# Kernel optimization log

Hardware: AMD Instinct MI355X
Metric: run time of the kernel (lower is better)

## Reference

```python
import jax, jax.numpy as jnp
import numpy as np

B, T, E = 2, 2048, 2048
H, NOPE, ROPE, VD, KVR, DR = 16, 64, 32, 64, 256, 2
QKD = NOPE + ROPE  # 96
LOWR = KVR // 4    # hypernet low_rank=4 -> 64


def _rope_angles(position, dim):
    # freqs_cis angles: pos * 10000^(-2i/dim), matching torch rotary with theta=10000
    inv = jnp.exp(jnp.arange(0, dim, 2, dtype=jnp.float32) * (-jnp.log(jnp.float32(10000.0)) / dim))
    return position.astype(jnp.float32)[..., None] * inv  # (1, T, dim//2)


def _apply_rotary(x, ang):
    # x: (B,T,H,D); pairs are consecutive elements (view_as_complex semantics)
    x2 = x.reshape(x.shape[:-1] + (-1, 2))
    c = jnp.cos(ang)[:, :, None, :]
    s = jnp.sin(ang)[:, :, None, :]
    xr, xi = x2[..., 0], x2[..., 1]
    return jnp.stack([xr * c - xi * s, xr * s + xi * c], axis=-1).reshape(x.shape)


def _layernorm(x, g, b, eps=1e-5):
    m = jnp.mean(x, axis=-1, keepdims=True)
    v = jnp.var(x, axis=-1, keepdims=True)
    return (x - m) * jax.lax.rsqrt(v + eps) * g + b


def _sinusoid_pe(t, d):
    pos = jnp.arange(t, dtype=jnp.float32)[:, None]
    div = jnp.exp(jnp.arange(0, d, 2, dtype=jnp.float32) * (-jnp.log(jnp.float32(10000.0)) / d))
    pe = jnp.zeros((t, d), dtype=jnp.float32)
    pe = pe.at[:, 0::2].set(jnp.sin(pos * div)).at[:, 1::2].set(jnp.cos(pos * div))
    return pe


def setup_inputs() -> dict:
    key = jax.random.key(0)
    ks = jax.random.split(key, 16)
    sd = 0.02
    return {
        "query": jax.random.normal(ks[0], (B, T, E), jnp.float32),
        "key": jax.random.normal(ks[1], (B, T, E), jnp.float32),
        "value": jax.random.normal(ks[2], (B, T, E), jnp.float32),
        "position": jnp.arange(T, dtype=jnp.int32)[None, :],
        # weights stored transposed for right-multiply (x @ W)
        "wq": jax.random.normal(ks[3], (E, H * QKD), jnp.float32) * sd,
        "wkv_a": jax.random.normal(ks[4], (E, KVR + ROPE), jnp.float32) * sd,
        "kv_gamma": jnp.ones((KVR,), jnp.float32),
        "kv_beta": jnp.zeros((KVR,), jnp.float32),
        # torch layout (H*(NOPE+VD), KVR) kept for faithful view(H,-1,KVR) absorb
        "wkv_b": jax.random.normal(ks[5], (H * (NOPE + VD), KVR), jnp.float32) * sd,
        "wo": jax.random.normal(ks[6], (H * VD, E), jnp.float32) * sd,
        "fc_c_w": jax.random.normal(ks[7], (KVR, LOWR), jnp.float32) * sd,
        "fc_c_b": jnp.zeros((LOWR,), jnp.float32),
        "fc_p_w": jax.random.normal(ks[8], (KVR, LOWR), jnp.float32) * sd,
        "fc_p_b": jnp.zeros((LOWR,), jnp.float32),
    }


def reference(query, key, value, position, wq, wkv_a, kv_gamma, kv_beta, wkv_b, wo,
              fc_c_w, fc_c_b, fc_p_w, fc_p_b):
    bsz, seqlen, _ = query.shape
    # queries: low-rank-free path (q_lora_rank=0)
    q = (query @ wq).reshape(bsz, seqlen, H, QKD)
    q_nope, q_pe = q[..., :NOPE], q[..., NOPE:]
    ang = _rope_angles(position, ROPE)  # (1, T, ROPE//2)
    q_pe = _apply_rotary(q_pe, ang[:, -seqlen:])
    # key/value latent projection
    kv_all = key @ wkv_a  # (B, T, KVR+ROPE)
    kv, k_pe = kv_all[..., :KVR], kv_all[..., KVR:]
    k_pe = _apply_rotary(k_pe[:, :, None, :], ang)[:, :, 0, :]  # (B, T, ROPE)
    kv_norm = _layernorm(kv, kv_gamma, kv_beta)  # (B, T, KVR)
    # hypernetwork temporal downsampling weights (train path, T_input=kv_norm)
    t = -(-seqlen // DR)
    C = jnp.repeat(_sinusoid_pe(t, KVR), DR, axis=0)[:seqlen]  # (T, KVR)
    C2 = C @ fc_c_w + fc_c_b           # (T, LOWR)
    P2 = kv_norm @ fc_p_w + fc_p_b     # (B, T, LOWR)
    W = jax.nn.sigmoid(jnp.einsum('tc,bsc->bts', C2, P2))  # (B, T, T)
    idx = jnp.arange(seqlen)
    chunk = idx // DR
    # chunk mask: cumulative within-chunk causal accumulation
    zero_mask = ((chunk[:, None] == chunk[None, :]) & (idx[None, :] <= idx[:, None])).astype(query.dtype)
    kv_t = jnp.einsum('bts,bsc->btc', W * zero_mask, kv_norm)  # (B, T, KVR)
    # stride-aware causal mask: attend completed chunk-end slots + own in-progress slot
    allowed = (idx[None, :] == idx[:, None]) | ((idx[None, :] < idx[:, None]) & (((idx[None, :] + 1) % DR) == 0))
    attn_mask = jnp.where(allowed, jnp.float32(0.0), jnp.float32(-1e30))
    # absorbed MLA attention
    wb = wkv_b.reshape(H, NOPE + VD, KVR)
    q_abs = jnp.einsum('bshd,hdc->bshc', q_nope, wb[:, :NOPE])  # (B, S, H, KVR)
    scores = (jnp.einsum('bshc,btc->bsht', q_abs, kv_t)
              + jnp.einsum('bshr,btr->bsht', q_pe, k_pe)) * (QKD ** -0.5)
    scores = scores + attn_mask[None, :, None, :]
    attn = jax.nn.softmax(scores, axis=-1)
    x = jnp.einsum('bsht,btc->bshc', attn, kv_t)
    x = jnp.einsum('bshc,hdc->bshd', x, wb[:, NOPE:])  # (B, S, H, VD)
    return x.reshape(bsz, seqlen, H * VD) @ wo
```

## Files before the change

kernel.cpp:

```cpp
#include <hip/hip_runtime.h>
#include <stddef.h>

typedef unsigned short u16;
typedef unsigned short u16x8 __attribute__((ext_vector_type(8)));
typedef short s16x8 __attribute__((ext_vector_type(8)));
typedef float f32x4 __attribute__((ext_vector_type(4)));

#define B_ 2
#define T_ 2048
#define E_ 2048
#define H_ 16

__device__ inline float us2f(u16 u){
  unsigned int i = ((unsigned int)u) << 16;
  return __builtin_bit_cast(float, i);
}
__device__ inline u16 f2us(float f){
  unsigned int x = __builtin_bit_cast(unsigned int, f);
  unsigned int r = (x + 0x7fffu + ((x >> 16) & 1u)) >> 16;
  return (u16)r;
}
__device__ inline f32x4 mfma32(s16x8 a, s16x8 b, f32x4 c){
  return __builtin_amdgcn_mfma_f32_16x16x32_bf16(a, b, c, 0, 0, 0);
}
__device__ inline s16x8 ld8(const u16* p){
  return __builtin_bit_cast(s16x8, *(const u16x8*)p);
}
__device__ inline void gload_lds16(const u16* g, u16* l){
  __builtin_amdgcn_global_load_lds(
      (const __attribute__((address_space(1))) unsigned int*)(g),
      (__attribute__((address_space(3))) unsigned int*)(l), 16, 0, 0);
}

__global__ __launch_bounds__(256) void prep_weights(
    const float* __restrict__ wq, const float* __restrict__ wkva,
    const float* __restrict__ wo, const float* __restrict__ wkvb,
    u16* __restrict__ wqT, u16* __restrict__ wkvaT, u16* __restrict__ woT,
    u16* __restrict__ wkvbB)
{
  __shared__ float tile[32][33];
  const int bid = blockIdx.x;
  const int tid = threadIdx.x;
  if (bid < 5696) {
    const float* in; u16* out; int R, C, bx, by;
    if (bid < 3072)      { in = wq;   out = wqT;   R = 2048; C = 1536; bx = bid % 48;          by = bid / 48; }
    else if (bid < 3648) { in = wkva; out = wkvaT; R = 2048; C = 288;  bx = (bid-3072) % 9;    by = (bid-3072) / 9; }
    else                 { in = wo;   out = woT;   R = 1024; C = 2048; bx = (bid-3648) % 64;   by = (bid-3648) / 64; }
    int tx = tid & 31, ty = tid >> 5;
    int c0 = bx * 32, r0 = by * 32;
    for (int i = ty; i < 32; i += 8){
      int r = r0 + i, c = c0 + tx;
      tile[i][tx] = (r < R && c < C) ? in[(size_t)r * C + c] : 0.f;
    }
    __syncthreads();
    for (int i = ty; i < 32; i += 8){
      int c = c0 + i, r = r0 + tx;
      if (c < C && r < R) out[(size_t)c * R + r] = f2us(tile[tx][i]);
    }
  } else {
    int i = (bid - 5696) * 1024 + tid * 4;
    f32x4 v = *(const f32x4*)(wkvb + i);
    wkvbB[i]   = f2us(v[0]); wkvbB[i+1] = f2us(v[1]);
    wkvbB[i+2] = f2us(v[2]); wkvbB[i+3] = f2us(v[3]);
  }
}

__global__ __launch_bounds__(256) void cvt2_f32_bf16(const float* __restrict__ a,
    const float* __restrict__ b, u16* __restrict__ oa, u16* __restrict__ ob, int n_each)
{
  int idx = (blockIdx.x * 256 + threadIdx.x) * 4;
  const float* in; u16* out; int i;
  if (idx < n_each){ in = a; out = oa; i = idx; }
  else             { in = b; out = ob; i = idx - n_each; }
  if (i + 3 < n_each){
    f32x4 v = *(const f32x4*)(in + i);
    out[i]   = f2us(v[0]); out[i+1] = f2us(v[1]);
    out[i+2] = f2us(v[2]); out[i+3] = f2us(v[3]);
  }
}

template<int A_F32, int OUT_F32>
__global__ __launch_bounds__(256) void gemm_bt(const void* __restrict__ Ap,
    const u16* __restrict__ Bt, void* __restrict__ Cp, int M, int N, int K)
{
  __shared__ __align__(16) u16 As[64][40];
  __shared__ __align__(16) u16 Bs[64][40];
  const int tid  = threadIdx.x;
  const int lane = tid & 63;
  const int wid  = tid >> 6;
  const int quad = lane >> 4;
  const int col  = lane & 15;
  const int bm = blockIdx.y * 64;
  const int bn = blockIdx.x * 64;
  const int lr = tid >> 2;
  const int lc = (tid & 3) * 8;
  const int waveM = wid >> 1, waveN = wid & 1;

  f32x4 acc[2][2];
  for (int i = 0; i < 2; ++i)
    for (int j = 0; j < 2; ++j)
      acc[i][j] = (f32x4){0.f, 0.f, 0.f, 0.f};

  const u16x8 zero8 = {0,0,0,0,0,0,0,0};
  const bool bok = (bn + lr) < N;
  const u16*   arow16 = (const u16*)Ap   + (size_t)(bm + lr) * K + lc;
  const float* arow32 = (const float*)Ap + (size_t)(bm + lr) * K + lc;
  const u16* brow = Bt + (size_t)(bn + lr) * K + lc;

  for (int kk = 0; kk < K; kk += 32) {
    u16x8 av;
    if (A_F32) {
      f32x4 a0 = *(const f32x4*)(arow32 + kk);
      f32x4 a1 = *(const f32x4*)(arow32 + kk + 4);
      av[0]=f2us(a0[0]); av[1]=f2us(a0[1]); av[2]=f2us(a0[2]); av[3]=f2us(a0[3]);
      av[4]=f2us(a1[0]); av[5]=f2us(a1[1]); av[6]=f2us(a1[2]); av[7]=f2us(a1[3]);
    } else {
      av = *(const u16x8*)(arow16 + kk);
    }
    u16x8 bv = bok ? *(const u16x8*)(brow + kk) : zero8;
    __syncthreads();
    *(u16x8*)&As[lr][lc] = av;
    *(u16x8*)&Bs[lr][lc] = bv;
    __syncthreads();
    s16x8 af0 = ld8(&As[waveM*32 + col][quad*8]);
    s16x8 af1 = ld8(&As[waveM*32 + 16 + col][quad*8]);
    s16x8 bf0 = ld8(&Bs[waveN*32 + col][quad*8]);
    s16x8 bf1 = ld8(&Bs[waveN*32 + 16 + col][quad*8]);
    acc[0][0] = mfma32(af0, bf0, acc[0][0]);
    acc[0][1] = mfma32(af0, bf1, acc[0][1]);
    acc[1][0] = mfma32(af1, bf0, acc[1][0]);
    acc[1][1] = mfma32(af1, bf1, acc[1][1]);
  }
  for (int am = 0; am < 2; ++am)
    for (int bnn = 0; bnn < 2; ++bnn)
      for (int i = 0; i < 4; ++i) {
        int r = bm + waveM*32 + am*16 + quad*4 + i;
        int c = bn + waveN*32 + bnn*16 + col;
        if (c < N){
          if (OUT_F32) ((float*)Cp)[(size_t)r * N + c] = acc[am][bnn][i];
          else         ((u16*)Cp)[(size_t)r * N + c]   = f2us(acc[am][bnn][i]);
        }
      }
}

template<int OUT_F32>
__global__ __launch_bounds__(256) void gemm128(const u16* __restrict__ A,
    const u16* __restrict__ Bt, void* __restrict__ Cp, int M, int N, int K, int gx)
{
  __shared__ __align__(16) u16 As[2 * 128 * 32];
  __shared__ __align__(16) u16 Bs[2 * 128 * 32];
  const int lin = blockIdx.x;
  const int cpx = gridDim.x >> 3;
  const int swz = (lin & 7) * cpx + (lin >> 3);
  const int bxi = swz % gx;
  const int byi = swz / gx;
  const int tid  = threadIdx.x;
  const int lane = tid & 63;
  const int wid  = tid >> 6;
  const int quad = lane >> 4;
  const int col  = lane & 15;
  const int bm = byi * 128;
  const int bn = bxi * 128;
  const int waveM = wid >> 1, waveN = wid & 1;

  const int srow = wid * 16 + (lane >> 2);
  const int scol = (lane & 3) * 8;
  const u16* ga = A  + (size_t)(bm + srow) * K + scol;
  const u16* gb = Bt + (size_t)(bn + srow) * K + scol;
  const size_t rowskip = (size_t)64 * K;

  f32x4 acc[4][4] = {};
  const int nt = K >> 5;

  auto STAGE = [&](int buf, int kk){
    u16* la = &As[buf * 4096 + wid * 512];
    u16* lb = &Bs[buf * 4096 + wid * 512];
    gload_lds16(ga + kk,           la);
    gload_lds16(ga + rowskip + kk, la + 2048);
    gload_lds16(gb + kk,           lb);
    gload_lds16(gb + rowskip + kk, lb + 2048);
  };

  STAGE(0, 0);
  asm volatile("s_waitcnt vmcnt(0)" ::: "memory");
  __builtin_amdgcn_s_barrier();
  __builtin_amdgcn_sched_barrier(0);

  int cur = 0;
  for (int it = 0; it < nt; ++it){
    if (it + 1 < nt) STAGE(cur ^ 1, (it + 1) * 32);
    const u16* as = &As[cur * 4096];
    const u16* bs = &Bs[cur * 4096];
    s16x8 af[4], bf[4];
#pragma unroll
    for (int i = 0; i < 4; ++i) af[i] = ld8(&as[(waveM*64 + i*16 + col) * 32 + quad*8]);
#pragma unroll
    for (int i = 0; i < 4; ++i) bf[i] = ld8(&bs[(waveN*64 + i*16 + col) * 32 + quad*8]);
#pragma unroll
    for (int i = 0; i < 4; ++i)
#pragma unroll
      for (int j = 0; j < 4; ++j)
        acc[i][j] = mfma32(af[i], bf[j], acc[i][j]);
    asm volatile("s_waitcnt lgkmcnt(0)" ::: "memory");
    if (it + 1 < nt)
      asm volatile("s_waitcnt vmcnt(0)" ::: "memory");
    __builtin_amdgcn_s_barrier();
    __builtin_amdgcn_sched_barrier(0);
    cur ^= 1;
  }
#pragma unroll
  for (int i = 0; i < 4; ++i)
#pragma unroll
    for (int j = 0; j < 4; ++j)
#pragma unroll
      for (int r = 0; r < 4; ++r) {
        int row = bm + waveM*64 + i*16 + quad*4 + r;
        int c   = bn + waveN*64 + j*16 + col;
        if (OUT_F32) ((float*)Cp)[(size_t)row * N + c] = acc[i][j][r];
        else         ((u16*)Cp)[(size_t)row * N + c]   = f2us(acc[i][j][r]);
      }
}

__global__ __launch_bounds__(256) void gemm128_sk(const u16* __restrict__ A,
    const u16* __restrict__ Bt, u16* __restrict__ qp,
    int M, int N, int K, int Klen)
{
  __shared__ __align__(16) u16 As[2 * 128 * 32];
  __shared__ __align__(16) u16 Bs[2 * 128 * 32];
  const int lin = blockIdx.x;
  const int swz = (lin & 7) * 96 + (lin >> 3);
  const int kh  = swz / 384;
  const int rem = swz % 384;
  const int byi = rem / 12;
  const int bxi = rem % 12;
  const int tid  = threadIdx.x;
  const int lane = tid & 63;
  const int wid  = tid >> 6;
  const int quad = lane >> 4;
  const int col  = lane & 15;
  const int bm = byi * 128;
  const int bn = bxi * 128;
  const int waveM = wid >> 1, waveN = wid & 1;

  const int srow = wid * 16 + (lane >> 2);
  const int scol = (lane & 3) * 8;
  const u16* ga = A  + (size_t)(bm + srow) * K + kh * Klen + scol;
  const u16* gb = Bt + (size_t)(bn + srow) * K + kh * Klen + scol;
  const size_t rowskip = (size_t)64 * K;
  u16* Cp = qp + (size_t)kh * M * N;

  f32x4 acc[4][4] = {};
  const int nt = Klen >> 5;

  auto STAGE = [&](int buf, int kk){
    u16* la = &As[buf * 4096 + wid * 512];
    u16* lb = &Bs[buf * 4096 + wid * 512];
    gload_lds16(ga + kk,           la);
    gload_lds16(ga + rowskip + kk, la + 2048);
    gload_lds16(gb + kk,           lb);
    gload_lds16(gb + rowskip + kk, lb + 2048);
  };

  STAGE(0, 0);
  asm volatile("s_waitcnt vmcnt(0)" ::: "memory");
  __builtin_amdgcn_s_barrier();
  __builtin_amdgcn_sched_barrier(0);

  int cur = 0;
  for (int it = 0; it < nt; ++it){
    if (it + 1 < nt) STAGE(cur ^ 1, (it + 1) * 32);
    const u16* as = &As[cur * 4096];
    const u16* bs = &Bs[cur * 4096];
    s16x8 af[4], bf[4];
#pragma unroll
    for (int i = 0; i < 4; ++i) af[i] = ld8(&as[(waveM*64 + i*16 + col) * 32 + quad*8]);
#pragma unroll
    for (int i = 0; i < 4; ++i) bf[i] = ld8(&bs[(waveN*64 + i*16 + col) * 32 + quad*8]);
#pragma unroll
    for (int i = 0; i < 4; ++i)
#pragma unroll
      for (int j = 0; j < 4; ++j)
        acc[i][j] = mfma32(af[i], bf[j], acc[i][j]);
    asm volatile("s_waitcnt lgkmcnt(0)" ::: "memory");
    if (it + 1 < nt)
      asm volatile("s_waitcnt vmcnt(0)" ::: "memory");
    __builtin_amdgcn_s_barrier();
    __builtin_amdgcn_sched_barrier(0);
    cur ^= 1;
  }
#pragma unroll
  for (int i = 0; i < 4; ++i)
#pragma unroll
    for (int j = 0; j < 4; ++j)
#pragma unroll
      for (int r = 0; r < 4; ++r) {
        int row = bm + waveM*64 + i*16 + quad*4 + r;
        int c   = bn + waveN*64 + j*16 + col;
        Cp[(size_t)row * N + c] = f2us(acc[i][j][r]);
      }
}

__global__ __launch_bounds__(256) void qsplit(const u16* __restrict__ qp,
    const int* __restrict__ pos, u16* __restrict__ qh)
{
  const size_t PS = 4096ull * 1536;
  int idx = blockIdx.x * 256 + threadIdx.x;
  if (idx >= B_*T_*H_*12) return;
  int c    = idx % 12;
  int rest = idx / 12;
  int h    = rest & 15;
  int row  = rest >> 4;
  int t    = row & (T_ - 1);
  int b    = row >> 11;
  size_t off = (size_t)row * 1536 + h * 96 + c * 8;
  u16x8 v0 = *(const u16x8*)(qp + off);
  u16x8 v1 = *(const u16x8*)(qp + PS + off);
  u16x8 v;
  if (c < 8) {
#pragma unroll
    for (int k = 0; k < 8; ++k) v[k] = f2us(us2f(v0[k]) + us2f(v1[k]));
  } else {
    int i0 = (c - 8) * 4;
    float pp = (float)pos[t];
#pragma unroll
    for (int k = 0; k < 4; ++k){
      int i = i0 + k;
      float ang = pp * __expf((float)(2*i) * -0.28782313657f);
      float cs = __cosf(ang), sn = __sinf(ang);
      float xr = us2f(v0[2*k])   + us2f(v1[2*k]);
      float xi = us2f(v0[2*k+1]) + us2f(v1[2*k+1]);
      v[2*k]   = f2us(xr * cs - xi * sn);
      v[2*k+1] = f2us(xr * sn + xi * cs);
    }
  }
  u16* dst = qh + ((size_t)(b * 16 + h) * T_ + t) * 96;
  *(u16x8*)(dst + c * 8) = v;
}

__global__ __launch_bounds__(256) void ln_p2_rope(
    const u16* __restrict__ kvall, const float* __restrict__ gamma,
    const float* __restrict__ beta, const float* __restrict__ fcpw,
    const float* __restrict__ fcpb, const int* __restrict__ pos,
    u16* __restrict__ kvn, float* __restrict__ P2, u16* __restrict__ kpe)
{
  const int row = blockIdx.x;
  if (row >= B_ * T_) return;
  const int tid = threadIdx.x;
  const int lane = tid & 63, wid = tid >> 6;
  __shared__ float kvs[256];
  __shared__ float part[256];
  __shared__ float redS[4], redS2[4];
  const u16* src = kvall + (size_t)row * 288;
  float v = us2f(src[tid]);
  float s1 = v, s2 = v * v;
  for (int off = 1; off < 64; off <<= 1){
    s1 += __shfl_xor(s1, off);
    s2 += __shfl_xor(s2, off);
  }
  if (lane == 0){ redS[wid] = s1; redS2[wid] = s2; }
  __syncthreads();
  float S  = redS[0] + redS[1] + redS[2] + redS[3];
  float Q  = redS2[0] + redS2[1] + redS2[2] + redS2[3];
  float mean = S * (1.f / 256.f);
  float var  = Q * (1.f / 256.f) - mean * mean;
  float rstd = rsqrtf(var + 1e-5f);
  float xn = (v - mean) * rstd * gamma[tid] + beta[tid];
  kvs[tid] = xn;
  kvn[(size_t)row * 256 + tid] = f2us(xn);
  __syncthreads();
  {
    int oc = tid & 63, pp = tid >> 6;
    float acc = 0.f;
#pragma unroll 8
    for (int c = pp * 64; c < pp * 64 + 64; ++c)
      acc += kvs[c] * fcpw[c * 64 + oc];
    part[tid] = acc;
  }
  __syncthreads();
  if (tid < 64) {
    P2[(size_t)row * 64 + tid] = fcpb[tid] + part[tid] + part[64 + tid]
                               + part[128 + tid] + part[192 + tid];
  } else if (tid < 80) {
    int i = tid - 64;
    int t = row & (T_ - 1);
    float ang = (float)pos[t] * __expf((float)(2*i) * -0.28782313657f);
    float c = __cosf(ang), s = __sinf(ang);
    float xr = us2f(src[256 + 2*i]);
    float xi = us2f(src[257 + 2*i]);
    kpe[(size_t)row * 32 + 2*i]     = f2us(xr * c - xi * s);
    kpe[(size_t)row * 32 + 2*i + 1] = f2us(xr * s + xi * c);
  }
}

__global__ __launch_bounds__(256) void c2_kernel(const float* __restrict__ fccw,
    const float* __restrict__ fccb, float* __restrict__ C2)
{
  const int t = blockIdx.x, tid = threadIdx.x;
  __shared__ float pe[256];
  __shared__ float part[256];
  float p = (float)(t >> 1);
  if (tid < 128){
    float div = __expf((float)(2*tid) * -0.03597789207f);
    float a = p * div;
    pe[2*tid]   = __sinf(a);
    pe[2*tid+1] = __cosf(a);
  }
  __syncthreads();
  {
    int oc = tid & 63, pp = tid >> 6;
    float acc = 0.f;
#pragma unroll 8
    for (int c = pp * 64; c < pp * 64 + 64; ++c)
      acc += pe[c] * fccw[c * 64 + oc];
    part[tid] = acc;
  }
  __syncthreads();
  if (tid < 64)
    C2[t * 64 + tid] = fccb[tid] + part[tid] + part[64 + tid]
                     + part[128 + tid] + part[192 + tid];
}

__global__ __launch_bounds__(64) void kvt_kernel(const float* __restrict__ C2,
    const float* __restrict__ P2, const u16* __restrict__ kvn, u16* __restrict__ kvt)
{
  const int row = blockIdx.x;
  if (row >= B_ * T_) return;
  const int lane = threadIdx.x;
  const int t = row & (T_ - 1);
  float c2v = C2[t * 64 + lane];
  float da = c2v * P2[(size_t)row * 64 + lane];
  for (int off = 1; off < 64; off <<= 1) da += __shfl_xor(da, off);
  float wtt = 1.f / (1.f + __expf(-da));
  const bool odd = (t & 1);
  float wts = 0.f;
  if (odd){
    float db = c2v * P2[(size_t)(row - 1) * 64 + lane];
    for (int off = 1; off < 64; off <<= 1) db += __shfl_xor(db, off);
    wts = 1.f / (1.f + __expf(-db));
  }
  for (int c = lane; c < 256; c += 64){
    float val = wtt * us2f(kvn[(size_t)row * 256 + c]);
    if (odd) val += wts * us2f(kvn[(size_t)(row - 1) * 256 + c]);
    kvt[(size_t)row * 256 + c] = f2us(val);
  }
}

__global__ __launch_bounds__(256) void vtkc_kernel(const u16* __restrict__ kvb,
    const u16* __restrict__ kpe, u16* __restrict__ Vt, u16* __restrict__ Kc)
{
  __shared__ __align__(16) u16 tile[64][72];
  const int tid = threadIdx.x;
  if (blockIdx.x < 512) {
    const int bid = blockIdx.x;
    const int jt = bid & 15;
    const int h  = (bid >> 4) & 15;
    const int b  = bid >> 8;
    const int jl = tid >> 2;
    const int dseg = (tid & 3) * 16;
    const int j0 = jt * 64;
    {
      int s_ = 2 * (j0 + jl) + 1;
      const u16* src = kvb + ((size_t)(b * T_ + s_)) * 2048 + h * 128 + 64 + dseg;
      *(u16x8*)&tile[jl][dseg]     = *(const u16x8*)(src);
      *(u16x8*)&tile[jl][dseg + 8] = *(const u16x8*)(src + 8);
    }
    __syncthreads();
    const int dl = tid >> 2;
    const int jseg = (tid & 3) * 16;
    u16* dst = Vt + ((size_t)(b * 16 + h) * 64 + dl) * 1024 + j0 + jseg;
    u16x8 o;
    for (int r = 0; r < 8; ++r) o[r] = tile[jseg + r][dl];
    *(u16x8*)dst = o;
    for (int r = 0; r < 8; ++r) o[r] = tile[jseg + 8 + r][dl];
    *(u16x8*)(dst + 8) = o;
  } else {
    int idx = (blockIdx.x - 512) * 256 + tid;
    int c  = idx % 12;
    int j  = (idx / 12) & 1023;
    int bh = idx / (12 * 1024);
    if (bh >= B_ * H_) return;
    int b = bh >> 4, h = bh & 15;
    int t = 2 * j + 1;
    u16x8 v;
    if (c < 8) v = *(const u16x8*)(kvb + ((size_t)(b * T_ + t)) * 2048 + h * 128 + c * 8);
    else       v = *(const u16x8*)(kpe + ((size_t)(b * T_ + t)) * 32 + (c - 8) * 8);
    int kl = j & 63;
    int cs = (c & 12) | ((c & 3) ^ ((kl >> 1) & 3));
    *(u16x8*)(Kc + ((size_t)bh * 1024 + j) * 96 + cs * 8) = v;
  }
}

__global__ __launch_bounds__(256) void attn_kernel(
    const u16* __restrict__ qh, const u16* __restrict__ kvb,
    const u16* __restrict__ kpe, const u16* __restrict__ Kc,
    const u16* __restrict__ Vt, u16* __restrict__ xout)
{
  __shared__ __align__(16) u16 Ks[64 * 96];
  __shared__ __align__(16) u16 Vs[64][72];
  __shared__ __align__(16) u16 pbufA[4][16 * 72];
  const int tid  = threadIdx.x;
  const int wid  = tid >> 6;
  const int lane = tid & 63;
  const int quad = lane >> 4;
  const int col  = lane & 15;
  const int qt   = 31 - (blockIdx.x >> 5);
  const int bh   = blockIdx.x & 31;
  const int b    = bh >> 4;
  const int h    = bh & 15;
  u16* pbuf = pbufA[wid];
  const float scale = 0.10206207262f;
  const u16* KcH = Kc + (size_t)bh * 1024 * 96;
  const u16* VtH = Vt + (size_t)bh * 64 * 1024;
  const int t0 = qt * 64 + wid * 16;
  const int qo = (quad * 8) ^ (((col >> 1) & 3) << 3);

  s16x8 aq0, aq1, aq2;
  {
    const u16* qrow = qh + ((size_t)bh * T_ + t0 + col) * 96;
    aq0 = ld8(qrow + quad * 8);
    aq1 = ld8(qrow + 32 + quad * 8);
    aq2 = ld8(qrow + 64 + quad * 8);
  }
  float sself;
  {
    const int t = t0 + col;
    const u16* qrow = qh + ((size_t)bh * T_ + t) * 96;
    const u16* ka = kvb + ((size_t)(b * T_ + t)) * 2048 + h * 128;
    const u16* kp = kpe + ((size_t)(b * T_ + t)) * 32;
    float a = 0.f;
#pragma unroll
    for (int c = 0; c < 8; ++c){
      u16x8 qv = *(const u16x8*)(qrow + c * 8);
      u16x8 kv = *(const u16x8*)(ka + c * 8);
#pragma unroll
      for (int jj = 0; jj < 8; ++jj) a += us2f(qv[jj]) * us2f(kv[jj]);
    }
#pragma unroll
    for (int c = 0; c < 4; ++c){
      u16x8 qv = *(const u16x8*)(qrow + 64 + c * 8);
      u16x8 kv = *(const u16x8*)(kp + c * 8);
#pragma unroll
      for (int jj = 0; jj < 8; ++jj) a += us2f(qv[jj]) * us2f(kv[jj]);
    }
    sself = a * scale;
  }
  float es[4], lacc[4];
  f32x4 O[4];
#pragma unroll
  for (int i = 0; i < 4; ++i){
    es[i] = __expf(__shfl(sself, quad * 4 + i));
    lacc[i] = 0.f;
  }
#pragma unroll
  for (int nt = 0; nt < 4; ++nt)
#pragma unroll
    for (int i = 0; i < 4; ++i){
      int t = t0 + quad * 4 + i;
      O[nt][i] = es[i] * us2f(kvb[((size_t)(b * T_ + t)) * 2048 + h * 128 + 64 + nt * 16 + col]);
    }

  const int nb = (qt * 32 + 94) >> 6;
  for (int blk = 0; blk < nb; ++blk) {
    const int jb = blk * 64;
    __syncthreads();
    {
      const u16* gk = KcH + (size_t)jb * 96 + (wid * 3) * 512 + lane * 8;
      u16* lk = &Ks[(wid * 3) * 512];
#pragma unroll
      for (int k = 0; k < 3; ++k)
        gload_lds16(gk + k * 512, lk + k * 512);
      int d = tid >> 2, c4 = tid & 3;
      const u16* gv = VtH + (size_t)d * 1024 + jb + c4 * 16;
      u16* lv = &Vs[d][c4 * 16];
      *(u16x8*)(lv)     = *(const u16x8*)(gv);
      *(u16x8*)(lv + 8) = *(const u16x8*)(gv + 8);
    }
    __syncthreads();
#pragma unroll
    for (int cc = 0; cc < 2; ++cc){
      const u16* k0 = &Ks[(cc * 32 + col) * 96];
      const u16* k1 = k0 + 16 * 96;
      f32x4 s0 = {0,0,0,0}, s1 = {0,0,0,0};
      s0 = mfma32(aq0, ld8(k0 + qo), s0);
      s0 = mfma32(aq1, ld8(k0 + 32 + qo), s0);
      s0 = mfma32(aq2, ld8(k0 + 64 + qo), s0);
      s1 = mfma32(aq0, ld8(k1 + qo), s1);
      s1 = mfma32(aq1, ld8(k1 + 32 + qo), s1);
      s1 = mfma32(aq2, ld8(k1 + 64 + qo), s1);
      int key0 = jb + cc * 32 + col;
#pragma unroll
      for (int i = 0; i < 4; ++i){
        int lim = (t0 + quad * 4 + i) >> 1;
        float p0 = (key0 < lim)      ? __expf(s0[i] * scale) : 0.f;
        float p1 = (key0 + 16 < lim) ? __expf(s1[i] * scale) : 0.f;
        lacc[i] += p0 + p1;
        pbuf[(quad * 4 + i) * 72 + cc * 32 + col]      = f2us(p0);
        pbuf[(quad * 4 + i) * 72 + cc * 32 + 16 + col] = f2us(p1);
      }
    }
    asm volatile("s_waitcnt lgkmcnt(0)" ::: "memory");
    __builtin_amdgcn_sched_barrier(0);
#pragma unroll
    for (int cc = 0; cc < 2; ++cc){
      s16x8 pf = ld8(&pbuf[col * 72 + cc * 32 + quad * 8]);
#pragma unroll
      for (int nt = 0; nt < 4; ++nt)
        O[nt] = mfma32(pf, ld8(&Vs[nt * 16 + col][cc * 32 + quad * 8]), O[nt]);
    }
  }
#pragma unroll
  for (int i = 0; i < 4; ++i){
    float l = lacc[i];
    l += __shfl_xor(l, 1);
    l += __shfl_xor(l, 2);
    l += __shfl_xor(l, 4);
    l += __shfl_xor(l, 8);
    lacc[i] = es[i] + l;
  }
#pragma unroll
  for (int nt = 0; nt < 4; ++nt)
#pragma unroll
    for (int i = 0; i < 4; ++i){
      int t = t0 + quad * 4 + i;
      xout[((size_t)(b * T_ + t)) * 1024 + h * 64 + nt * 16 + col] = f2us(O[nt][i] / lacc[i]);
    }
}

extern "C" void kernel_launch(void* const* d_in, const int* in_sizes, int n_in,
                              void* d_out, int out_size, void* d_ws, size_t ws_size,
                              hipStream_t stream)
{
  (void)in_sizes; (void)n_in; (void)out_size; (void)ws_size;
  const float* query = (const float*)d_in[0];
  const float* key_  = (const float*)d_in[1];
  const int*   pos   = (const int*)d_in[3];
  const float* wq    = (const float*)d_in[4];
  const float* wkva  = (const float*)d_in[5];
  const float* gamma = (const float*)d_in[6];
  const float* beta  = (const float*)d_in[7];
  const float* wkvb  = (const float*)d_in[8];
  const float* wo    = (const float*)d_in[9];
  const float* fccw  = (const float*)d_in[10];
  const float* fccb  = (const float*)d_in[11];
  const float* fcpw  = (const float*)d_in[12];
  const float* fcpb  = (const float*)d_in[13];

  char* p = (char*)d_ws;
  auto alloc = [&](size_t bytes) -> void* {
    void* r = (void*)p;
    p += (bytes + 255) & ~(size_t)255;
    return r;
  };
  u16* wqT    = (u16*)alloc(1536ull * 2048 * 2);
  u16* wkvaT  = (u16*)alloc(288ull  * 2048 * 2);
  u16* woT    = (u16*)alloc(2048ull * 1024 * 2);
  u16* wkvbB  = (u16*)alloc(2048ull * 256 * 2);
  u16* queryB = (u16*)alloc(4096ull * 2048 * 2);
  u16* keyB   = (u16*)alloc(4096ull * 2048 * 2);
  u16* qp     = (u16*)alloc(2ull * 4096 * 1536 * 2);
  u16* qh     = (u16*)alloc(65536ull * 96 * 2);
  u16* kvall  = (u16*)alloc(4096ull * 288 * 2);
  u16* kvn    = (u16*)alloc(4096ull * 256 * 2);
  u16* kpe    = (u16*)alloc(4096ull * 32 * 2);
  float* P2   = (float*)alloc(4096ull * 64 * 4);
  float* C2   = (float*)alloc(2048ull * 64 * 4);
  u16* kvt    = (u16*)alloc(4096ull * 256 * 2);
  u16* kvb    = (u16*)alloc(4096ull * 2048 * 2);
  char* q8 = (char*)qp;
  u16* Kc = (u16*)q8;
  u16* Vt = (u16*)(q8 + ((32ull*1024*96*2 + 255) & ~255ull));
  u16* x  = (u16*)(q8 + ((32ull*1024*96*2 + 255) & ~255ull)
                      + ((2048ull*1024*2   + 255) & ~255ull));

  prep_weights<<<6208, 256, 0, stream>>>(wq, wkva, wo, wkvb, wqT, wkvaT, woT, wkvbB);
  cvt2_f32_bf16<<<16384, 256, 0, stream>>>(query, key_, queryB, keyB, 4096 * 2048);

  gemm128_sk<<<768, 256, 0, stream>>>(queryB, wqT, qp, 4096, 1536, 2048, 1024);
  gemm_bt<0,0><<<dim3(5, 64), 256, 0, stream>>>(keyB, wkvaT, kvall, 4096, 288, 2048);

  qsplit<<<3072, 256, 0, stream>>>(qp, pos, qh);
  ln_p2_rope<<<4096, 256, 0, stream>>>(kvall, gamma, beta, fcpw, fcpb, pos, kvn, P2, kpe);
  c2_kernel<<<2048, 256, 0, stream>>>(fccw, fccb, C2);
  kvt_kernel<<<4096, 64, 0, stream>>>(C2, P2, kvn, kvt);

  gemm128<0><<<512, 256, 0, stream>>>(kvt, wkvbB, kvb, 4096, 2048, 256, 16);
  vtkc_kernel<<<2048, 256, 0, stream>>>(kvb, kpe, Vt, Kc);
  attn_kernel<<<1024, 256, 0, stream>>>(qh, kvb, kpe, Kc, Vt, x);

  gemm128<1><<<512, 256, 0, stream>>>(x, woT, d_out, 4096, 2048, 1024, 16);
}
```

Before: 347.2 us.

## Merge independent prep, projection and mid-stage kernels into combined launches

Independent kernels are merged into fewer launches by dispatching on block index. Weight prep joins the query/key conversion, the Q split-K GEMM joins the small kv_a GEMM, and qsplit, LayerNorm/P2/RoPE and C2 share one kernel. kvt_kernel now packs four rows per 256-thread block. This cuts launch overhead and lets small, under-filled kernels overlap on the GPU, at the cost of heterogeneous blocks sharing resource limits such as LDS sized for the largest branch.

```diff
diff --git a/kernel.cpp b/kernel.cpp
--- a/kernel.cpp
+++ b/kernel.cpp
@@ -32,11 +32,12 @@
       (__attribute__((address_space(3))) unsigned int*)(l), 16, 0, 0);
 }
 
-__global__ __launch_bounds__(256) void prep_weights(
+__global__ __launch_bounds__(256) void prep_cvt(
     const float* __restrict__ wq, const float* __restrict__ wkva,
     const float* __restrict__ wo, const float* __restrict__ wkvb,
+    const float* __restrict__ query, const float* __restrict__ key_,
     u16* __restrict__ wqT, u16* __restrict__ wkvaT, u16* __restrict__ woT,
-    u16* __restrict__ wkvbB)
+    u16* __restrict__ wkvbB, u16* __restrict__ queryB, u16* __restrict__ keyB)
 {
   __shared__ float tile[32][33];
   const int bid = blockIdx.x;
@@ -57,90 +58,149 @@
       int c = c0 + i, r = r0 + tx;
       if (c < C && r < R) out[(size_t)c * R + r] = f2us(tile[tx][i]);
     }
-  } else {
+  } else if (bid < 6208) {
     int i = (bid - 5696) * 1024 + tid * 4;
     f32x4 v = *(const f32x4*)(wkvb + i);
     wkvbB[i]   = f2us(v[0]); wkvbB[i+1] = f2us(v[1]);
     wkvbB[i+2] = f2us(v[2]); wkvbB[i+3] = f2us(v[3]);
-  }
-}
-
-__global__ __launch_bounds__(256) void cvt2_f32_bf16(const float* __restrict__ a,
-    const float* __restrict__ b, u16* __restrict__ oa, u16* __restrict__ ob, int n_each)
-{
-  int idx = (blockIdx.x * 256 + threadIdx.x) * 4;
-  const float* in; u16* out; int i;
-  if (idx < n_each){ in = a; out = oa; i = idx; }
-  else             { in = b; out = ob; i = idx - n_each; }
-  if (i + 3 < n_each){
-    f32x4 v = *(const f32x4*)(in + i);
-    out[i]   = f2us(v[0]); out[i+1] = f2us(v[1]);
-    out[i+2] = f2us(v[2]); out[i+3] = f2us(v[3]);
-  }
-}
-
-template<int A_F32, int OUT_F32>
-__global__ __launch_bounds__(256) void gemm_bt(const void* __restrict__ Ap,
-    const u16* __restrict__ Bt, void* __restrict__ Cp, int M, int N, int K)
-{
-  __shared__ __align__(16) u16 As[64][40];
-  __shared__ __align__(16) u16 Bs[64][40];
+  } else {
+    const int n_each = 4096 * 2048;
+    int idx = (bid - 6208) * 1024 + tid * 4;
+    const float* in; u16* out; int i;
+    if (idx < n_each){ in = query; out = queryB; i = idx; }
+    else             { in = key_;  out = keyB;   i = idx - n_each; }
+    if (i + 3 < n_each){
+      f32x4 v = *(const f32x4*)(in + i);
+      out[i]   = f2us(v[0]); out[i+1] = f2us(v[1]);
+      out[i+2] = f2us(v[2]); out[i+3] = f2us(v[3]);
+    }
+  }
+}
+
+__global__ __launch_bounds__(256) void proj2(
+    const u16* __restrict__ queryB, const u16* __restrict__ wqT, u16* __restrict__ qp,
+    const u16* __restrict__ keyB, const u16* __restrict__ wkvaT, u16* __restrict__ kvall)
+{
+  __shared__ __align__(16) u16 smem[16384];
+  const int bid = blockIdx.x;
   const int tid  = threadIdx.x;
   const int lane = tid & 63;
   const int wid  = tid >> 6;
   const int quad = lane >> 4;
   const int col  = lane & 15;
-  const int bm = blockIdx.y * 64;
-  const int bn = blockIdx.x * 64;
-  const int lr = tid >> 2;
-  const int lc = (tid & 3) * 8;
-  const int waveM = wid >> 1, waveN = wid & 1;
-
-  f32x4 acc[2][2];
-  for (int i = 0; i < 2; ++i)
-    for (int j = 0; j < 2; ++j)
-      acc[i][j] = (f32x4){0.f, 0.f, 0.f, 0.f};
-
-  const u16x8 zero8 = {0,0,0,0,0,0,0,0};
-  const bool bok = (bn + lr) < N;
-  const u16*   arow16 = (const u16*)Ap   + (size_t)(bm + lr) * K + lc;
-  const float* arow32 = (const float*)Ap + (size_t)(bm + lr) * K + lc;
-  const u16* brow = Bt + (size_t)(bn + lr) * K + lc;
-
-  for (int kk = 0; kk < K; kk += 32) {
-    u16x8 av;
-    if (A_F32) {
-      f32x4 a0 = *(const f32x4*)(arow32 + kk);
-      f32x4 a1 = *(const f32x4*)(arow32 + kk + 4);
-      av[0]=f2us(a0[0]); av[1]=f2us(a0[1]); av[2]=f2us(a0[2]); av[3]=f2us(a0[3]);
-      av[4]=f2us(a1[0]); av[5]=f2us(a1[1]); av[6]=f2us(a1[2]); av[7]=f2us(a1[3]);
-    } else {
-      av = *(const u16x8*)(arow16 + kk);
-    }
-    u16x8 bv = bok ? *(const u16x8*)(brow + kk) : zero8;
-    __syncthreads();
-    *(u16x8*)&As[lr][lc] = av;
-    *(u16x8*)&Bs[lr][lc] = bv;
-    __syncthreads();
-    s16x8 af0 = ld8(&As[waveM*32 + col][quad*8]);
-    s16x8 af1 = ld8(&As[waveM*32 + 16 + col][quad*8]);
-    s16x8 bf0 = ld8(&Bs[waveN*32 + col][quad*8]);
-    s16x8 bf1 = ld8(&Bs[waveN*32 + 16 + col][quad*8]);
-    acc[0][0] = mfma32(af0, bf0, acc[0][0]);
-    acc[0][1] = mfma32(af0, bf1, acc[0][1]);
-    acc[1][0] = mfma32(af1, bf0, acc[1][0]);
-    acc[1][1] = mfma32(af1, bf1, acc[1][1]);
-  }
-  for (int am = 0; am < 2; ++am)
-    for (int bnn = 0; bnn < 2; ++bnn)
-      for (int i = 0; i < 4; ++i) {
-        int r = bm + waveM*32 + am*16 + quad*4 + i;
-        int c = bn + waveN*32 + bnn*16 + col;
-        if (c < N){
-          if (OUT_F32) ((float*)Cp)[(size_t)r * N + c] = acc[am][bnn][i];
-          else         ((u16*)Cp)[(size_t)r * N + c]   = f2us(acc[am][bnn][i]);
+
+  if (bid < 768) {
+    const int N = 1536, K = 2048, Klen = 1024;
+    const int swz = (bid & 7) * 96 + (bid >> 3);
+    const int kh  = swz / 384;
+    const int rem = swz % 384;
+    const int bm = (rem / 12) * 128;
+    const int bn = (rem % 12) * 128;
+    const int waveM = wid >> 1, waveN = wid & 1;
+    u16* As = smem;
+    u16* Bs = smem + 8192;
+
+    const int srow = wid * 16 + (lane >> 2);
+    const int scol = (lane & 3) * 8;
+    const u16* ga = queryB + (size_t)(bm + srow) * K + kh * Klen + scol;
+    const u16* gb = wqT    + (size_t)(bn + srow) * K + kh * Klen + scol;
+    const size_t rowskip = (size_t)64 * K;
+    u16* Cp = qp + (size_t)kh * 4096 * N;
+
+    f32x4 acc[4][4] = {};
+    const int nt = Klen >> 5;
+
+    auto STAGE = [&](int buf, int kk){
+      u16* la = &As[buf * 4096 + wid * 512];
+      u16* lb = &Bs[buf * 4096 + wid * 512];
+      gload_lds16(ga + kk,           la);
+      gload_lds16(ga + rowskip + kk, la + 2048);
+      gload_lds16(gb + kk,           lb);
+      gload_lds16(gb + rowskip + kk, lb + 2048);
+    };
+
+    STAGE(0, 0);
+    asm volatile("s_waitcnt vmcnt(0)" ::: "memory");
+    __builtin_amdgcn_s_barrier();
+    __builtin_amdgcn_sched_barrier(0);
+
+    int cur = 0;
+    for (int it = 0; it < nt; ++it){
+      if (it + 1 < nt) STAGE(cur ^ 1, (it + 1) * 32);
+      const u16* as = &As[cur * 4096];
+      const u16* bs = &Bs[cur * 4096];
+      s16x8 af[4], bf[4];
+#pragma unroll
+      for (int i = 0; i < 4; ++i) af[i] = ld8(&as[(waveM*64 + i*16 + col) * 32 + quad*8]);
+#pragma unroll
+      for (int i = 0; i < 4; ++i) bf[i] = ld8(&bs[(waveN*64 + i*16 + col) * 32 + quad*8]);
+#pragma unroll
+      for (int i = 0; i < 4; ++i)
+#pragma unroll
+        for (int j = 0; j < 4; ++j)
+          acc[i][j] = mfma32(af[i], bf[j], acc[i][j]);
+      asm volatile("s_waitcnt lgkmcnt(0)" ::: "memory");
+      if (it + 1 < nt)
+        asm volatile("s_waitcnt vmcnt(0)" ::: "memory");
+      __builtin_amdgcn_s_barrier();
+      __builtin_amdgcn_sched_barrier(0);
+      cur ^= 1;
+    }
+#pragma unroll
+    for (int i = 0; i < 4; ++i)
+#pragma unroll
+      for (int j = 0; j < 4; ++j)
+#pragma unroll
+        for (int r = 0; r < 4; ++r) {
+          int row = bm + waveM*64 + i*16 + quad*4 + r;
+          int c   = bn + waveN*64 + j*16 + col;
+          Cp[(size_t)row * N + c] = f2us(acc[i][j][r]);
         }
-      }
+  } else {
+    const int N = 288, K = 2048;
+    const int r_ = bid - 768;
+    const int bm = (r_ / 5) * 64;
+    const int bn = (r_ % 5) * 64;
+    const int lr = tid >> 2;
+    const int lc = (tid & 3) * 8;
+    const int waveM = wid >> 1, waveN = wid & 1;
+    u16* As = smem;
+    u16* Bs = smem + 2560;
+
+    f32x4 acc[2][2];
+    for (int i = 0; i < 2; ++i)
+      for (int j = 0; j < 2; ++j)
+        acc[i][j] = (f32x4){0.f, 0.f, 0.f, 0.f};
+
+    const u16x8 zero8 = {0,0,0,0,0,0,0,0};
+    const bool bok = (bn + lr) < N;
+    const u16* arow = keyB  + (size_t)(bm + lr) * K + lc;
+    const u16* brow = wkvaT + (size_t)(bn + lr) * K + lc;
+
+    for (int kk = 0; kk < K; kk += 32) {
+      u16x8 av = *(const u16x8*)(arow + kk);
+      u16x8 bv = bok ? *(const u16x8*)(brow + kk) : zero8;
+      __syncthreads();
+      *(u16x8*)&As[lr*40 + lc] = av;
+      *(u16x8*)&Bs[lr*40 + lc] = bv;
+      __syncthreads();
+      s16x8 af0 = ld8(&As[(waveM*32 + col)*40 + quad*8]);
+      s16x8 af1 = ld8(&As[(waveM*32 + 16 + col)*40 + quad*8]);
+      s16x8 bf0 = ld8(&Bs[(waveN*32 + col)*40 + quad*8]);
+      s16x8 bf1 = ld8(&Bs[(waveN*32 + 16 + col)*40 + quad*8]);
+      acc[0][0] = mfma32(af0, bf0, acc[0][0]);
+      acc[0][1] = mfma32(af0, bf1, acc[0][1]);
+      acc[1][0] = mfma32(af1, bf0, acc[1][0]);
+      acc[1][1] = mfma32(af1, bf1, acc[1][1]);
+    }
+    for (int am = 0; am < 2; ++am)
+      for (int bnn = 0; bnn < 2; ++bnn)
+        for (int i = 0; i < 4; ++i) {
+          int r = bm + waveM*32 + am*16 + quad*4 + i;
+          int c = bn + waveN*32 + bnn*16 + col;
+          if (c < N) kvall[(size_t)r * N + c] = f2us(acc[am][bnn][i]);
+        }
+  }
 }
 
 template<int OUT_F32>
@@ -221,211 +281,130 @@
       }
 }
 
-__global__ __launch_bounds__(256) void gemm128_sk(const u16* __restrict__ A,
-    const u16* __restrict__ Bt, u16* __restrict__ qp,
-    int M, int N, int K, int Klen)
-{
-  __shared__ __align__(16) u16 As[2 * 128 * 32];
-  __shared__ __align__(16) u16 Bs[2 * 128 * 32];
-  const int lin = blockIdx.x;
-  const int swz = (lin & 7) * 96 + (lin >> 3);
-  const int kh  = swz / 384;
-  const int rem = swz % 384;
-  const int byi = rem / 12;
-  const int bxi = rem % 12;
-  const int tid  = threadIdx.x;
-  const int lane = tid & 63;
-  const int wid  = tid >> 6;
-  const int quad = lane >> 4;
-  const int col  = lane & 15;
-  const int bm = byi * 128;
-  const int bn = bxi * 128;
-  const int waveM = wid >> 1, waveN = wid & 1;
-
-  const int srow = wid * 16 + (lane >> 2);
-  const int scol = (lane & 3) * 8;
-  const u16* ga = A  + (size_t)(bm + srow) * K + kh * Klen + scol;
-  const u16* gb = Bt + (size_t)(bn + srow) * K + kh * Klen + scol;
-  const size_t rowskip = (size_t)64 * K;
-  u16* Cp = qp + (size_t)kh * M * N;
-
-  f32x4 acc[4][4] = {};
-  const int nt = Klen >> 5;
-
-  auto STAGE = [&](int buf, int kk){
-    u16* la = &As[buf * 4096 + wid * 512];
-    u16* lb = &Bs[buf * 4096 + wid * 512];
-    gload_lds16(ga + kk,           la);
-    gload_lds16(ga + rowskip + kk, la + 2048);
-    gload_lds16(gb + kk,           lb);
-    gload_lds16(gb + rowskip + kk, lb + 2048);
-  };
-
-  STAGE(0, 0);
-  asm volatile("s_waitcnt vmcnt(0)" ::: "memory");
-  __builtin_amdgcn_s_barrier();
-  __builtin_amdgcn_sched_barrier(0);
-
-  int cur = 0;
-  for (int it = 0; it < nt; ++it){
-    if (it + 1 < nt) STAGE(cur ^ 1, (it + 1) * 32);
-    const u16* as = &As[cur * 4096];
-    const u16* bs = &Bs[cur * 4096];
-    s16x8 af[4], bf[4];
-#pragma unroll
-    for (int i = 0; i < 4; ++i) af[i] = ld8(&as[(waveM*64 + i*16 + col) * 32 + quad*8]);
-#pragma unroll
-    for (int i = 0; i < 4; ++i) bf[i] = ld8(&bs[(waveN*64 + i*16 + col) * 32 + quad*8]);
-#pragma unroll
-    for (int i = 0; i < 4; ++i)
-#pragma unroll
-      for (int j = 0; j < 4; ++j)
-        acc[i][j] = mfma32(af[i], bf[j], acc[i][j]);
-    asm volatile("s_waitcnt lgkmcnt(0)" ::: "memory");
-    if (it + 1 < nt)
-      asm volatile("s_waitcnt vmcnt(0)" ::: "memory");
-    __builtin_amdgcn_s_barrier();
-    __builtin_amdgcn_sched_barrier(0);
-    cur ^= 1;
-  }
-#pragma unroll
-  for (int i = 0; i < 4; ++i)
-#pragma unroll
-    for (int j = 0; j < 4; ++j)
-#pragma unroll
-      for (int r = 0; r < 4; ++r) {
-        int row = bm + waveM*64 + i*16 + quad*4 + r;
-        int c   = bn + waveN*64 + j*16 + col;
-        Cp[(size_t)row * N + c] = f2us(acc[i][j][r]);
-      }
-}
-
-__global__ __launch_bounds__(256) void qsplit(const u16* __restrict__ qp,
-    const int* __restrict__ pos, u16* __restrict__ qh)
-{
-  const size_t PS = 4096ull * 1536;
-  int idx = blockIdx.x * 256 + threadIdx.x;
-  if (idx >= B_*T_*H_*12) return;
-  int c    = idx % 12;
-  int rest = idx / 12;
-  int h    = rest & 15;
-  int row  = rest >> 4;
-  int t    = row & (T_ - 1);
-  int b    = row >> 11;
-  size_t off = (size_t)row * 1536 + h * 96 + c * 8;
-  u16x8 v0 = *(const u16x8*)(qp + off);
-  u16x8 v1 = *(const u16x8*)(qp + PS + off);
-  u16x8 v;
-  if (c < 8) {
-#pragma unroll
-    for (int k = 0; k < 8; ++k) v[k] = f2us(us2f(v0[k]) + us2f(v1[k]));
-  } else {
-    int i0 = (c - 8) * 4;
-    float pp = (float)pos[t];
-#pragma unroll
-    for (int k = 0; k < 4; ++k){
-      int i = i0 + k;
-      float ang = pp * __expf((float)(2*i) * -0.28782313657f);
-      float cs = __cosf(ang), sn = __sinf(ang);
-      float xr = us2f(v0[2*k])   + us2f(v1[2*k]);
-      float xi = us2f(v0[2*k+1]) + us2f(v1[2*k+1]);
-      v[2*k]   = f2us(xr * cs - xi * sn);
-      v[2*k+1] = f2us(xr * sn + xi * cs);
-    }
-  }
-  u16* dst = qh + ((size_t)(b * 16 + h) * T_ + t) * 96;
-  *(u16x8*)(dst + c * 8) = v;
-}
-
-__global__ __launch_bounds__(256) void ln_p2_rope(
+__global__ __launch_bounds__(256) void mid3(
+    const u16* __restrict__ qp, const int* __restrict__ pos, u16* __restrict__ qh,
     const u16* __restrict__ kvall, const float* __restrict__ gamma,
     const float* __restrict__ beta, const float* __restrict__ fcpw,
-    const float* __restrict__ fcpb, const int* __restrict__ pos,
-    u16* __restrict__ kvn, float* __restrict__ P2, u16* __restrict__ kpe)
-{
-  const int row = blockIdx.x;
-  if (row >= B_ * T_) return;
+    const float* __restrict__ fcpb, u16* __restrict__ kvn,
+    float* __restrict__ P2, u16* __restrict__ kpe,
+    const float* __restrict__ fccw, const float* __restrict__ fccb,
+    float* __restrict__ C2)
+{
+  __shared__ float fsm[520];
+  const int bid = blockIdx.x;
   const int tid = threadIdx.x;
-  const int lane = tid & 63, wid = tid >> 6;
-  __shared__ float kvs[256];
-  __shared__ float part[256];
-  __shared__ float redS[4], redS2[4];
-  const u16* src = kvall + (size_t)row * 288;
-  float v = us2f(src[tid]);
-  float s1 = v, s2 = v * v;
-  for (int off = 1; off < 64; off <<= 1){
-    s1 += __shfl_xor(s1, off);
-    s2 += __shfl_xor(s2, off);
-  }
-  if (lane == 0){ redS[wid] = s1; redS2[wid] = s2; }
-  __syncthreads();
-  float S  = redS[0] + redS[1] + redS[2] + redS[3];
-  float Q  = redS2[0] + redS2[1] + redS2[2] + redS2[3];
-  float mean = S * (1.f / 256.f);
-  float var  = Q * (1.f / 256.f) - mean * mean;
-  float rstd = rsqrtf(var + 1e-5f);
-  float xn = (v - mean) * rstd * gamma[tid] + beta[tid];
-  kvs[tid] = xn;
-  kvn[(size_t)row * 256 + tid] = f2us(xn);
-  __syncthreads();
-  {
-    int oc = tid & 63, pp = tid >> 6;
-    float acc = 0.f;
+
+  if (bid < 3072) {
+    const size_t PS = 4096ull * 1536;
+    int idx = bid * 256 + tid;
+    int c    = idx % 12;
+    int rest = idx / 12;
+    int h    = rest & 15;
+    int row  = rest >> 4;
+    int t    = row & (T_ - 1);
+    int b    = row >> 11;
+    size_t off = (size_t)row * 1536 + h * 96 + c * 8;
+    u16x8 v0 = *(const u16x8*)(qp + off);
+    u16x8 v1 = *(const u16x8*)(qp + PS + off);
+    u16x8 v;
+    if (c < 8) {
+#pragma unroll
+      for (int k = 0; k < 8; ++k) v[k] = f2us(us2f(v0[k]) + us2f(v1[k]));
+    } else {
+      int i0 = (c - 8) * 4;
+      float pp = (float)pos[t];
+#pragma unroll
+      for (int k = 0; k < 4; ++k){
+        int i = i0 + k;
+        float ang = pp * __expf((float)(2*i) * -0.28782313657f);
+        float cs = __cosf(ang), sn = __sinf(ang);
+        float xr = us2f(v0[2*k])   + us2f(v1[2*k]);
+        float xi = us2f(v0[2*k+1]) + us2f(v1[2*k+1]);
+        v[2*k]   = f2us(xr * cs - xi * sn);
+        v[2*k+1] = f2us(xr * sn + xi * cs);
+      }
+    }
+    u16* dst = qh + ((size_t)(b * 16 + h) * T_ + t) * 96;
+    *(u16x8*)(dst + c * 8) = v;
+  } else if (bid < 7168) {
+    const int row = bid - 3072;
+    const int lane = tid & 63, wid = tid >> 6;
+    float* kvs   = fsm;
+    float* part  = fsm + 256;
+    float* redS  = fsm + 512;
+    float* redS2 = fsm + 516;
+    const u16* src = kvall + (size_t)row * 288;
+    float v = us2f(src[tid]);
+    float s1 = v, s2 = v * v;
+    for (int off = 1; off < 64; off <<= 1){
+      s1 += __shfl_xor(s1, off);
+      s2 += __shfl_xor(s2, off);
+    }
+    if (lane == 0){ redS[wid] = s1; redS2[wid] = s2; }
+    __syncthreads();
+    float S  = redS[0] + redS[1] + redS[2] + redS[3];
+    float Q  = redS2[0] + redS2[1] + redS2[2] + redS2[3];
+    float mean = S * (1.f / 256.f);
+    float var  = Q * (1.f / 256.f) - mean * mean;
+    float rstd = rsqrtf(var + 1e-5f);
+    float xn = (v - mean) * rstd * gamma[tid] + beta[tid];
+    kvs[tid] = xn;
+    kvn[(size_t)row * 256 + tid] = f2us(xn);
+    __syncthreads();
+    {
+      int oc = tid & 63, pp = tid >> 6;
+      float acc = 0.f;
 #pragma unroll 8
-    for (int c = pp * 64; c < pp * 64 + 64; ++c)
-      acc += kvs[c] * fcpw[c * 64 + oc];
-    part[tid] = acc;
-  }
-  __syncthreads();
-  if (tid < 64) {
-    P2[(size_t)row * 64 + tid] = fcpb[tid] + part[tid] + part[64 + tid]
-                               + part[128 + tid] + part[192 + tid];
-  } else if (tid < 80) {
-    int i = tid - 64;
-    int t = row & (T_ - 1);
-    float ang = (float)pos[t] * __expf((float)(2*i) * -0.28782313657f);
-    float c = __cosf(ang), s = __sinf(ang);
-    float xr = us2f(src[256 + 2*i]);
-    float xi = us2f(src[257 + 2*i]);
-    kpe[(size_t)row * 32 + 2*i]     = f2us(xr * c - xi * s);
-    kpe[(size_t)row * 32 + 2*i + 1] = f2us(xr * s + xi * c);
-  }
-}
-
-__global__ __launch_bounds__(256) void c2_kernel(const float* __restrict__ fccw,
-    const float* __restrict__ fccb, float* __restrict__ C2)
-{
-  const int t = blockIdx.x, tid = threadIdx.x;
-  __shared__ float pe[256];
-  __shared__ float part[256];
-  float p = (float)(t >> 1);
-  if (tid < 128){
-    float div = __expf((float)(2*tid) * -0.03597789207f);
-    float a = p * div;
-    pe[2*tid]   = __sinf(a);
-    pe[2*tid+1] = __cosf(a);
-  }
-  __syncthreads();
-  {
-    int oc = tid & 63, pp = tid >> 6;
-    float acc = 0.f;
+      for (int c = pp * 64; c < pp * 64 + 64; ++c)
+        acc += kvs[c] * fcpw[c * 64 + oc];
+      part[tid] = acc;
+    }
+    __syncthreads();
+    if (tid < 64) {
+      P2[(size_t)row * 64 + tid] = fcpb[tid] + part[tid] + part[64 + tid]
+                                 + part[128 + tid] + part[192 + tid];
+    } else if (tid < 80) {
+      int i = tid - 64;
+      int t = row & (T_ - 1);
+      float ang = (float)pos[t] * __expf((float)(2*i) * -0.28782313657f);
+      float c = __cosf(ang), s = __sinf(ang);
+      float xr = us2f(src[256 + 2*i]);
+      float xi = us2f(src[257 + 2*i]);
+      kpe[(size_t)row * 32 + 2*i]     = f2us(xr * c - xi * s);
+      kpe[(size_t)row * 32 + 2*i + 1] = f2us(xr * s + xi * c);
+    }
+  } else {
+    const int t = bid - 7168;
+    float* pe   = fsm;
+    float* part = fsm + 256;
+    float p = (float)(t >> 1);
+    if (tid < 128){
+      float div = __expf((float)(2*tid) * -0.03597789207f);
+      float a = p * div;
+      pe[2*tid]   = __sinf(a);
+      pe[2*tid+1] = __cosf(a);
+    }
+    __syncthreads();
+    {
+      int oc = tid & 63, pp = tid >> 6;
+      float acc = 0.f;
 #pragma unroll 8
-    for (int c = pp * 64; c < pp * 64 + 64; ++c)
-      acc += pe[c] * fccw[c * 64 + oc];
-    part[tid] = acc;
-  }
-  __syncthreads();
-  if (tid < 64)
-    C2[t * 64 + tid] = fccb[tid] + part[tid] + part[64 + tid]
-                     + part[128 + tid] + part[192 + tid];
-}
-
-__global__ __launch_bounds__(64) void kvt_kernel(const float* __restrict__ C2,
+      for (int c = pp * 64; c < pp * 64 + 64; ++c)
+        acc += pe[c] * fccw[c * 64 + oc];
+      part[tid] = acc;
+    }
+    __syncthreads();
+    if (tid < 64)
+      C2[t * 64 + tid] = fccb[tid] + part[tid] + part[64 + tid]
+                       + part[128 + tid] + part[192 + tid];
+  }
+}
+
+__global__ __launch_bounds__(256) void kvt_kernel(const float* __restrict__ C2,
     const float* __restrict__ P2, const u16* __restrict__ kvn, u16* __restrict__ kvt)
 {
-  const int row = blockIdx.x;
-  if (row >= B_ * T_) return;
-  const int lane = threadIdx.x;
+  const int row = blockIdx.x * 4 + (threadIdx.x >> 6);
+  const int lane = threadIdx.x & 63;
   const int t = row & (T_ - 1);
   float c2v = C2[t * 64 + lane];
   float da = c2v * P2[(size_t)row * 64 + lane];
@@ -672,16 +651,12 @@
   u16* x  = (u16*)(q8 + ((32ull*1024*96*2 + 255) & ~255ull)
                       + ((2048ull*1024*2   + 255) & ~255ull));
 
-  prep_weights<<<6208, 256, 0, stream>>>(wq, wkva, wo, wkvb, wqT, wkvaT, woT, wkvbB);
-  cvt2_f32_bf16<<<16384, 256, 0, stream>>>(query, key_, queryB, keyB, 4096 * 2048);
-
-  gemm128_sk<<<768, 256, 0, stream>>>(queryB, wqT, qp, 4096, 1536, 2048, 1024);
-  gemm_bt<0,0><<<dim3(5, 64), 256, 0, stream>>>(keyB, wkvaT, kvall, 4096, 288, 2048);
-
-  qsplit<<<3072, 256, 0, stream>>>(qp, pos, qh);
-  ln_p2_rope<<<4096, 256, 0, stream>>>(kvall, gamma, beta, fcpw, fcpb, pos, kvn, P2, kpe);
-  c2_kernel<<<2048, 256, 0, stream>>>(fccw, fccb, C2);
-  kvt_kernel<<<4096, 64, 0, stream>>>(C2, P2, kvn, kvt);
+  prep_cvt<<<22592, 256, 0, stream>>>(wq, wkva, wo, wkvb, query, key_,
+                                      wqT, wkvaT, woT, wkvbB, queryB, keyB);
+  proj2<<<1088, 256, 0, stream>>>(queryB, wqT, qp, keyB, wkvaT, kvall);
+  mid3<<<9216, 256, 0, stream>>>(qp, pos, qh, kvall, gamma, beta, fcpw, fcpb,
+                                 kvn, P2, kpe, fccw, fccb, C2);
+  kvt_kernel<<<1024, 256, 0, stream>>>(C2, P2, kvn, kvt);
 
   gemm128<0><<<512, 256, 0, stream>>>(kvt, wkvbB, kvb, 4096, 2048, 256, 16);
   vtkc_kernel<<<2048, 256, 0, stream>>>(kvb, kpe, Vt, Kc);
```

New measurement: 337.3 us. -2.9%, faster.
